# Kernel tuning notes

Measured on AMD Instinct MI355X. Metric: run time of the kernel, lower is better.

## Reference

```python
import jax, jax.numpy as jnp
import numpy as np

D_MODEL = 1024
N_HEADS = 16
HEAD_DIM = D_MODEL // N_HEADS
NEG_INF = -1e10


def setup_inputs() -> dict:
    key = jax.random.key(0)
    ks = jax.random.split(key, 6)
    B, S = 2, 2048
    x = jax.random.normal(ks[0], (B, S, D_MODEL), dtype=jnp.float32)
    mask = jnp.ones((B, S), dtype=jnp.int32)
    scale_w = 1.0 / np.sqrt(D_MODEL)
    Wq = jax.random.normal(ks[1], (D_MODEL, D_MODEL), dtype=jnp.float32) * scale_w
    Wk = jax.random.normal(ks[2], (D_MODEL, D_MODEL), dtype=jnp.float32) * scale_w
    Wv = jax.random.normal(ks[3], (D_MODEL, D_MODEL), dtype=jnp.float32) * scale_w
    Wo = jax.random.normal(ks[4], (D_MODEL, D_MODEL), dtype=jnp.float32) * scale_w
    bq = jnp.zeros((D_MODEL,), jnp.float32)
    bk = jnp.zeros((D_MODEL,), jnp.float32)
    bv = jnp.zeros((D_MODEL,), jnp.float32)
    bo = jnp.zeros((D_MODEL,), jnp.float32)
    return {"x": x, "mask": mask, "Wq": Wq, "bq": bq, "Wk": Wk, "bk": bk,
            "Wv": Wv, "bv": bv, "Wo": Wo, "bo": bo}


def reference(x, mask, Wq, bq, Wk, bk, Wv, bv, Wo, bo):
    B, S, _ = x.shape
    # Linear projections (torch Linear: y = x @ W.T + b)
    Q = x @ Wq.T + bq
    K = x @ Wk.T + bk
    V = x @ Wv.T + bv
    # [B, H, S, Dh]
    Q = Q.reshape(B, S, N_HEADS, HEAD_DIM).transpose(0, 2, 1, 3)
    K = K.reshape(B, S, N_HEADS, HEAD_DIM).transpose(0, 2, 1, 3)
    V = V.reshape(B, S, N_HEADS, HEAD_DIM).transpose(0, 2, 1, 3)
    scale = jnp.sqrt(jnp.float32(HEAD_DIM))
    energy = jnp.einsum('bhqd,bhkd->bhqk', Q, K) / scale  # [B,H,S,S]
    # mask: [B,S] -> broadcast over heads and query dim (keys masked)
    m = mask[:, None, None, :]  # [B,1,1,S]
    energy = jnp.where(m == 0, jnp.float32(NEG_INF), energy)
    attention = jax.nn.softmax(energy, axis=-1)
    # dropout in eval mode = identity
    out = jnp.einsum('bhqk,bhkd->bhqd', attention, V)  # [B,H,S,Dh]
    out = out.transpose(0, 2, 1, 3).reshape(B, S, D_MODEL)
    return out @ Wo.T + bo
```

## Files before the change

kernel.cpp:

```cpp
#include <hip/hip_runtime.h>
#include <hip/hip_bf16.h>

typedef __hip_bfloat16 bf16;
typedef __attribute__((ext_vector_type(8))) short s8v;
typedef __attribute__((ext_vector_type(4))) float f4v;

#define D_MODEL 1024
#define S_LEN   2048
#define BATCH   2
#define NH      16
#define HD      64
#define M_TOTAL 4096

__device__ __forceinline__ void gll16(const bf16* g, bf16* l) {
    __builtin_amdgcn_global_load_lds(
        (const __attribute__((address_space(1))) void*)g,
        (__attribute__((address_space(3))) void*)l, 16, 0, 0);
}

__global__ __launch_bounds__(256) void cvt_bf16x8(const float* __restrict__ s,
                                                  bf16* __restrict__ d, int n) {
    int i = (blockIdx.x * 256 + threadIdx.x) * 8;
    if (i < n) {
        float4 a = *(const float4*)(s + i);
        float4 b = *(const float4*)(s + i + 4);
        union { bf16 h[8]; uint4 u; } p;
        p.h[0] = __float2bfloat16(a.x); p.h[1] = __float2bfloat16(a.y);
        p.h[2] = __float2bfloat16(a.z); p.h[3] = __float2bfloat16(a.w);
        p.h[4] = __float2bfloat16(b.x); p.h[5] = __float2bfloat16(b.y);
        p.h[6] = __float2bfloat16(b.z); p.h[7] = __float2bfloat16(b.w);
        *(uint4*)(d + i) = p.u;
    }
}

struct WPtrs { const float* s0; const float* s1; const float* s2; const float* s3;
               bf16* d0; bf16* d1; bf16* d2; bf16* d3; };

__global__ __launch_bounds__(256) void cvt_w(WPtrs p) {
    const float* s; bf16* d;
    switch (blockIdx.y) {
        case 0:  s = p.s0; d = p.d0; break;
        case 1:  s = p.s1; d = p.d1; break;
        case 2:  s = p.s2; d = p.d2; break;
        default: s = p.s3; d = p.d3; break;
    }
    int i = (blockIdx.x * 256 + threadIdx.x) * 8;
    float4 a = *(const float4*)(s + i);
    float4 b = *(const float4*)(s + i + 4);
    union { bf16 h[8]; uint4 u; } q;
    q.h[0] = __float2bfloat16(a.x); q.h[1] = __float2bfloat16(a.y);
    q.h[2] = __float2bfloat16(a.z); q.h[3] = __float2bfloat16(a.w);
    q.h[4] = __float2bfloat16(b.x); q.h[5] = __float2bfloat16(b.y);
    q.h[6] = __float2bfloat16(b.z); q.h[7] = __float2bfloat16(b.w);
    *(uint4*)(d + i) = q.u;
}

template<int TM, int TN>
__device__ __forceinline__ void gemm_main(const bf16* __restrict__ A,
                                          const bf16* __restrict__ W,
                                          bf16* As, bf16* Bs,
                                          int bm, int bn,
                                          f4v (&acc)[TM/32][TN/32])
{
    constexpr int FM = TM / 32, FN = TN / 32;
    constexpr int CALLS_A = TM / 16, CALLS = (TM + TN) / 16, PW = CALLS / 4;
    const int t = threadIdx.x, wv = t >> 6, lane = t & 63;
    const int quad = lane >> 4, l15 = lane & 15;
    const int wm = (wv >> 1) * (TM / 2), wn = (wv & 1) * (TN / 2);
    const int lr = lane >> 2, lc = (lane & 3) * 8;

    const bf16* aptr[FM];
    const bf16* bptr[FN];
    #pragma unroll
    for (int i = 0; i < FM; ++i) aptr[i] = As + (wm + i * 16 + l15) * 32 + quad * 8;
    #pragma unroll
    for (int j = 0; j < FN; ++j) bptr[j] = Bs + (wn + j * 16 + l15) * 32 + quad * 8;

    for (int k0 = 0; k0 < D_MODEL; k0 += 32) {
        __syncthreads();
        #pragma unroll
        for (int c = 0; c < PW; ++c) {
            const int cc = wv * PW + c;
            if (cc < CALLS_A) {
                gll16(A + (size_t)(bm + cc * 16 + lr) * D_MODEL + k0 + lc,
                      As + cc * 16 * 32);
            } else {
                const int r2 = cc - CALLS_A;
                gll16(W + (size_t)(bn + r2 * 16 + lr) * D_MODEL + k0 + lc,
                      Bs + r2 * 16 * 32);
            }
        }
        __syncthreads();

        s8v af[FM], bfv[FN];
        #pragma unroll
        for (int i = 0; i < FM; ++i) af[i] = *(const s8v*)aptr[i];
        #pragma unroll
        for (int j = 0; j < FN; ++j) bfv[j] = *(const s8v*)bptr[j];
        #pragma unroll
        for (int i = 0; i < FM; ++i)
            #pragma unroll
            for (int j = 0; j < FN; ++j)
                acc[i][j] = __builtin_amdgcn_mfma_f32_16x16x32_bf16(af[i], bfv[j], acc[i][j], 0, 0, 0);
    }
}

__global__ __launch_bounds__(256) void gemm_qkv(
    const bf16* __restrict__ x,
    const bf16* __restrict__ Wq, const bf16* __restrict__ Wk, const bf16* __restrict__ Wv,
    const float* __restrict__ bq, const float* __restrict__ bk, const float* __restrict__ bv,
    bf16* __restrict__ Qb, bf16* __restrict__ Kb, bf16* __restrict__ Vtb)
{
    __shared__ __align__(16) bf16 As[128 * 32];
    __shared__ __align__(16) bf16 Bs[128 * 32];
    const int z = blockIdx.z;
    const bf16*  W    = (z == 0) ? Wq : (z == 1) ? Wk : Wv;
    const float* bias = (z == 0) ? bq : (z == 1) ? bk : bv;
    bf16*        out  = (z == 0) ? Qb : (z == 1) ? Kb : Vtb;
    const int bm = blockIdx.y * 128, bn = blockIdx.x * 128;

    f4v acc[4][4] = {};
    gemm_main<128, 128>(x, W, As, Bs, bm, bn, acc);

    const int t = threadIdx.x, wv = t >> 6, lane = t & 63;
    const int quad = lane >> 4, l15 = lane & 15;
    const int wm = (wv >> 1) * 64, wn = (wv & 1) * 64;
    #pragma unroll
    for (int j = 0; j < 4; ++j) {
        const int col = bn + wn + j * 16 + l15;
        const float bv_ = bias[col];
        const int h = col >> 6, d = col & 63;
        #pragma unroll
        for (int i = 0; i < 4; ++i) {
            #pragma unroll
            for (int r = 0; r < 4; ++r) {
                const int row = bm + wm + i * 16 + quad * 4 + r;
                const int b = row >> 11, s = row & 2047;
                const float v = acc[i][j][r] + bv_;
                size_t idx;
                if (z == 2) idx = (((size_t)(b * NH + h)) * HD + d) * S_LEN + s;
                else        idx = (((size_t)(b * NH + h)) * S_LEN + s) * HD + d;
                out[idx] = __float2bfloat16(v);
            }
        }
    }
}

__global__ __launch_bounds__(256) void gemm_out(
    const bf16* __restrict__ Ob, const bf16* __restrict__ Wo,
    const float* __restrict__ bo, float* __restrict__ out)
{
    __shared__ __align__(16) bf16 As[64 * 32];
    __shared__ __align__(16) bf16 Bs[128 * 32];
    const int bm = blockIdx.y * 64, bn = blockIdx.x * 128;

    f4v acc[2][4] = {};
    gemm_main<64, 128>(Ob, Wo, As, Bs, bm, bn, acc);

    const int t = threadIdx.x, wv = t >> 6, lane = t & 63;
    const int quad = lane >> 4, l15 = lane & 15;
    const int wm = (wv >> 1) * 32, wn = (wv & 1) * 64;
    #pragma unroll
    for (int j = 0; j < 4; ++j) {
        const int col = bn + wn + j * 16 + l15;
        const float bv_ = bo[col];
        #pragma unroll
        for (int i = 0; i < 2; ++i)
            #pragma unroll
            for (int r = 0; r < 4; ++r) {
                const int row = bm + wm + i * 16 + quad * 4 + r;
                out[(size_t)row * D_MODEL + col] = acc[i][j][r] + bv_;
            }
    }
}

__global__ __launch_bounds__(256) void attn_mfma(
    const bf16* __restrict__ Q, const bf16* __restrict__ K,
    const bf16* __restrict__ Vt, const int* __restrict__ mask,
    bf16* __restrict__ O)
{
    __shared__ __align__(16) bf16 Ks[64][72];
    __shared__ __align__(16) bf16 Vts[64][72];
    __shared__ __align__(16) bf16 Ps[4][16][72];
    __shared__ __align__(16) int  msk[64];

    const int t = threadIdx.x, wv = t >> 6, lane = t & 63;
    const int quad = lane >> 4, l15 = lane & 15;
    const int qt = blockIdx.x & 31, h = (blockIdx.x >> 5) & 15, b = blockIdx.x >> 9;
    const int q0 = qt * 64;
    const size_t qkbase = ((size_t)(b * NH + h)) * S_LEN * HD;
    const size_t vtbase = ((size_t)(b * NH + h)) * HD * S_LEN;

    const bf16* qrow = Q + qkbase + (size_t)(q0 + wv * 16 + l15) * HD;
    const s8v qf0 = *(const s8v*)(qrow + quad * 8);
    const s8v qf1 = *(const s8v*)(qrow + 32 + quad * 8);

    const int srow = t >> 2, scoff = (t & 3) * 16;

    float mprev = -1e30f, lsum = 0.f;
    f4v oacc[4] = {};

    for (int kt = 0; kt < S_LEN / 64; ++kt) {
        const int k0 = kt * 64;
        __syncthreads();
        {
            const uint4* kp = (const uint4*)(K  + qkbase + (size_t)(k0 + srow) * HD + scoff);
            const uint4* vp = (const uint4*)(Vt + vtbase + (size_t)srow * S_LEN + k0 + scoff);
            uint4 ka = kp[0], kb2 = kp[1];
            uint4 va = vp[0], vb2 = vp[1];
            *(uint4*)&Ks[srow][scoff]      = ka;
            *(uint4*)&Ks[srow][scoff + 8]  = kb2;
            *(uint4*)&Vts[srow][scoff]     = va;
            *(uint4*)&Vts[srow][scoff + 8] = vb2;
            if (t < 64) msk[t] = mask[b * S_LEN + k0 + t];
        }
        __syncthreads();

        f4v st[4];
        #pragma unroll
        for (int c = 0; c < 4; ++c) {
            s8v kf0 = *(const s8v*)&Ks[c * 16 + l15][quad * 8];
            s8v kf1 = *(const s8v*)&Ks[c * 16 + l15][32 + quad * 8];
            f4v z = {0.f, 0.f, 0.f, 0.f};
            z = __builtin_amdgcn_mfma_f32_16x16x32_bf16(kf0, qf0, z, 0, 0, 0);
            z = __builtin_amdgcn_mfma_f32_16x16x32_bf16(kf1, qf1, z, 0, 0, 0);
            st[c] = z;
        }

        float mt = -1e30f;
        #pragma unroll
        for (int c = 0; c < 4; ++c) {
            const int4 mk = *(const int4*)&msk[c * 16 + quad * 4];
            float v0 = st[c][0] * 0.125f; if (mk.x == 0) v0 = -1e10f;
            float v1 = st[c][1] * 0.125f; if (mk.y == 0) v1 = -1e10f;
            float v2 = st[c][2] * 0.125f; if (mk.z == 0) v2 = -1e10f;
            float v3 = st[c][3] * 0.125f; if (mk.w == 0) v3 = -1e10f;
            st[c][0] = v0; st[c][1] = v1; st[c][2] = v2; st[c][3] = v3;
            mt = fmaxf(mt, fmaxf(fmaxf(v0, v1), fmaxf(v2, v3)));
        }
        mt = fmaxf(mt, __shfl_xor(mt, 16, 64));
        mt = fmaxf(mt, __shfl_xor(mt, 32, 64));

        const float mn = fmaxf(mprev, mt);
        const float alpha = __expf(mprev - mn);
        mprev = mn;

        float ps = 0.f;
        #pragma unroll
        for (int c = 0; c < 4; ++c) {
            #pragma unroll
            for (int r = 0; r < 4; ++r) {
                const float p = __expf(st[c][r] - mn);
                st[c][r] = p;
                ps += p;
            }
        }
        ps += __shfl_xor(ps, 16, 64);
        ps += __shfl_xor(ps, 32, 64);
        lsum = lsum * alpha + ps;

        #pragma unroll
        for (int c = 0; c < 4; ++c) {
            union { bf16 h[4]; short4 s4; } pk;
            pk.h[0] = __float2bfloat16(st[c][0]);
            pk.h[1] = __float2bfloat16(st[c][1]);
            pk.h[2] = __float2bfloat16(st[c][2]);
            pk.h[3] = __float2bfloat16(st[c][3]);
            *(short4*)&Ps[wv][l15][c * 16 + quad * 4] = pk.s4;
        }

        float av[4];
        #pragma unroll
        for (int r = 0; r < 4; ++r) av[r] = __shfl(alpha, quad * 4 + r, 64);
        #pragma unroll
        for (int dt = 0; dt < 4; ++dt)
            #pragma unroll
            for (int r = 0; r < 4; ++r) oacc[dt][r] *= av[r];

        s8v pf0 = *(const s8v*)&Ps[wv][l15][quad * 8];
        s8v pf1 = *(const s8v*)&Ps[wv][l15][32 + quad * 8];
        #pragma unroll
        for (int dt = 0; dt < 4; ++dt) {
            s8v vf0 = *(const s8v*)&Vts[dt * 16 + l15][quad * 8];
            s8v vf1 = *(const s8v*)&Vts[dt * 16 + l15][32 + quad * 8];
            oacc[dt] = __builtin_amdgcn_mfma_f32_16x16x32_bf16(pf0, vf0, oacc[dt], 0, 0, 0);
            oacc[dt] = __builtin_amdgcn_mfma_f32_16x16x32_bf16(pf1, vf1, oacc[dt], 0, 0, 0);
        }
    }

    float linv[4];
    #pragma unroll
    for (int r = 0; r < 4; ++r) linv[r] = 1.f / __shfl(lsum, quad * 4 + r, 64);
    #pragma unroll
    for (int dt = 0; dt < 4; ++dt) {
        #pragma unroll
        for (int r = 0; r < 4; ++r) {
            const int s = q0 + wv * 16 + quad * 4 + r;
            const int col = h * 64 + dt * 16 + l15;
            O[((size_t)b * S_LEN + s) * D_MODEL + col] = __float2bfloat16(oacc[dt][r] * linv[r]);
        }
    }
}

extern "C" void kernel_launch(void* const* d_in, const int* in_sizes, int n_in,
                              void* d_out, int out_size, void* d_ws, size_t ws_size,
                              hipStream_t stream) {
    const float* x    = (const float*)d_in[0];
    const int*   mask = (const int*)  d_in[1];
    const float* Wq   = (const float*)d_in[2];
    const float* bq   = (const float*)d_in[3];
    const float* Wk   = (const float*)d_in[4];
    const float* bk   = (const float*)d_in[5];
    const float* Wv   = (const float*)d_in[6];
    const float* bv   = (const float*)d_in[7];
    const float* Wo   = (const float*)d_in[8];
    const float* bo   = (const float*)d_in[9];
    float* out = (float*)d_out;

    char* w = (char*)d_ws;
    bf16* xb  = (bf16*)w; w += (size_t)M_TOTAL * D_MODEL * 2;
    bf16* Wqb = (bf16*)w; w += (size_t)D_MODEL * D_MODEL * 2;
    bf16* Wkb = (bf16*)w; w += (size_t)D_MODEL * D_MODEL * 2;
    bf16* Wvb = (bf16*)w; w += (size_t)D_MODEL * D_MODEL * 2;
    bf16* Wob = (bf16*)w; w += (size_t)D_MODEL * D_MODEL * 2;
    bf16* Qb  = (bf16*)w; w += (size_t)M_TOTAL * D_MODEL * 2;
    bf16* Kb  = (bf16*)w; w += (size_t)M_TOTAL * D_MODEL * 2;
    bf16* Vtb = (bf16*)w; w += (size_t)M_TOTAL * D_MODEL * 2;
    bf16* Ob  = (bf16*)w; w += (size_t)M_TOTAL * D_MODEL * 2;

    const int nx = M_TOTAL * D_MODEL;
    cvt_bf16x8<<<nx / 2048, 256, 0, stream>>>(x, xb, nx);
    WPtrs wp = { Wq, Wk, Wv, Wo, Wqb, Wkb, Wvb, Wob };
    cvt_w<<<dim3(D_MODEL * D_MODEL / 2048, 4), 256, 0, stream>>>(wp);

    gemm_qkv<<<dim3(8, 32, 3), 256, 0, stream>>>(xb, Wqb, Wkb, Wvb, bq, bk, bv, Qb, Kb, Vtb);

    attn_mfma<<<BATCH * NH * (S_LEN / 64), 256, 0, stream>>>(Qb, Kb, Vtb, mask, Ob);

    gemm_out<<<dim3(8, 64), 256, 0, stream>>>(Ob, Wob, bo, out);
}
```

Before: 242.3 us.

## Prefetch K/V tiles, use exp2 with lazy rescaling, transpose V stores via LDS

The attention loop now loads the next K/V tile into registers while the current tile is being computed. The softmax folds log2(e) into the scale and uses exp2, turns the mask into an additive bias, and skips the rescale when the running max barely changes. Row-sum reductions are deferred until after the loop, and s_setprio is raised around the MFMA blocks. Separately, the V-transpose epilogue of the QKV GEMM is staged through LDS so global writes become coalesced 16-byte stores; this adds extra LDS use, which may lower occupancy.

New measurement: 233.2 us. -3.8%, faster.

```diff
diff --git a/kernel.cpp b/kernel.cpp
--- a/kernel.cpp
+++ b/kernel.cpp
@@ -113,6 +113,7 @@
 {
     __shared__ __align__(16) bf16 As[128 * 32];
     __shared__ __align__(16) bf16 Bs[128 * 32];
+    __shared__ __align__(16) bf16 Tw[4][64][72];
     const int z = blockIdx.z;
     const bf16*  W    = (z == 0) ? Wq : (z == 1) ? Wk : Wv;
     const float* bias = (z == 0) ? bq : (z == 1) ? bk : bv;
@@ -125,22 +126,48 @@
     const int t = threadIdx.x, wv = t >> 6, lane = t & 63;
     const int quad = lane >> 4, l15 = lane & 15;
     const int wm = (wv >> 1) * 64, wn = (wv & 1) * 64;
-    #pragma unroll
-    for (int j = 0; j < 4; ++j) {
-        const int col = bn + wn + j * 16 + l15;
-        const float bv_ = bias[col];
-        const int h = col >> 6, d = col & 63;
-        #pragma unroll
-        for (int i = 0; i < 4; ++i) {
-            #pragma unroll
-            for (int r = 0; r < 4; ++r) {
-                const int row = bm + wm + i * 16 + quad * 4 + r;
-                const int b = row >> 11, s = row & 2047;
-                const float v = acc[i][j][r] + bv_;
-                size_t idx;
-                if (z == 2) idx = (((size_t)(b * NH + h)) * HD + d) * S_LEN + s;
-                else        idx = (((size_t)(b * NH + h)) * S_LEN + s) * HD + d;
-                out[idx] = __float2bfloat16(v);
+
+    if (z == 2) {
+        #pragma unroll
+        for (int j = 0; j < 4; ++j) {
+            const int col = bn + wn + j * 16 + l15;
+            const float bv_ = bias[col];
+            #pragma unroll
+            for (int i = 0; i < 4; ++i) {
+                #pragma unroll
+                for (int rp = 0; rp < 4; rp += 2) {
+                    union { bf16 h[2]; unsigned u; } p2;
+                    p2.h[0] = __float2bfloat16(acc[i][j][rp]     + bv_);
+                    p2.h[1] = __float2bfloat16(acc[i][j][rp + 1] + bv_);
+                    *(unsigned*)&Tw[wv][j * 16 + l15][i * 16 + quad * 4 + rp] = p2.u;
+                }
+            }
+        }
+        const int bb = (bm + wm) >> 11, s0 = (bm + wm) & 2047;
+        #pragma unroll
+        for (int p = 0; p < 8; ++p) {
+            const int dl = p * 8 + (lane >> 3);
+            const int sl = (lane & 7) * 8;
+            const int col = bn + wn + dl;
+            const int h = col >> 6, d = col & 63;
+            uint4 v = *(const uint4*)&Tw[wv][dl][sl];
+            *(uint4*)&out[(((size_t)(bb * NH + h)) * HD + d) * S_LEN + s0 + sl] = v;
+        }
+    } else {
+        #pragma unroll
+        for (int j = 0; j < 4; ++j) {
+            const int col = bn + wn + j * 16 + l15;
+            const float bv_ = bias[col];
+            const int h = col >> 6, d = col & 63;
+            #pragma unroll
+            for (int i = 0; i < 4; ++i) {
+                #pragma unroll
+                for (int r = 0; r < 4; ++r) {
+                    const int row = bm + wm + i * 16 + quad * 4 + r;
+                    const int b = row >> 11, s = row & 2047;
+                    const float v = acc[i][j][r] + bv_;
+                    out[(((size_t)(b * NH + h)) * S_LEN + s) * HD + d] = __float2bfloat16(v);
+                }
             }
         }
     }
@@ -182,7 +209,7 @@
     __shared__ __align__(16) bf16 Ks[64][72];
     __shared__ __align__(16) bf16 Vts[64][72];
     __shared__ __align__(16) bf16 Ps[4][16][72];
-    __shared__ __align__(16) int  msk[64];
+    __shared__ float mb[64];
 
     const int t = threadIdx.x, wv = t >> 6, lane = t & 63;
     const int quad = lane >> 4, l15 = lane & 15;
@@ -191,32 +218,41 @@
     const size_t qkbase = ((size_t)(b * NH + h)) * S_LEN * HD;
     const size_t vtbase = ((size_t)(b * NH + h)) * HD * S_LEN;
 
+    const float KSC  = 0.125f * 1.44269504f;
+    const float THR2 = 8.0f * 1.44269504f;
+
     const bf16* qrow = Q + qkbase + (size_t)(q0 + wv * 16 + l15) * HD;
     const s8v qf0 = *(const s8v*)(qrow + quad * 8);
     const s8v qf1 = *(const s8v*)(qrow + 32 + quad * 8);
 
     const int srow = t >> 2, scoff = (t & 3) * 16;
 
+    uint4 kr0, kr1, vr0, vr1; int mr = 1;
+    auto LOADT = [&](int kt2) {
+        const int kk = kt2 * 64;
+        const uint4* kp = (const uint4*)(K  + qkbase + (size_t)(kk + srow) * HD + scoff);
+        const uint4* vp = (const uint4*)(Vt + vtbase + (size_t)srow * S_LEN + kk + scoff);
+        kr0 = kp[0]; kr1 = kp[1];
+        vr0 = vp[0]; vr1 = vp[1];
+        if (t < 64) mr = mask[b * S_LEN + kk + t];
+    };
+    LOADT(0);
+
     float mprev = -1e30f, lsum = 0.f;
     f4v oacc[4] = {};
 
     for (int kt = 0; kt < S_LEN / 64; ++kt) {
-        const int k0 = kt * 64;
         __syncthreads();
-        {
-            const uint4* kp = (const uint4*)(K  + qkbase + (size_t)(k0 + srow) * HD + scoff);
-            const uint4* vp = (const uint4*)(Vt + vtbase + (size_t)srow * S_LEN + k0 + scoff);
-            uint4 ka = kp[0], kb2 = kp[1];
-            uint4 va = vp[0], vb2 = vp[1];
-            *(uint4*)&Ks[srow][scoff]      = ka;
-            *(uint4*)&Ks[srow][scoff + 8]  = kb2;
-            *(uint4*)&Vts[srow][scoff]     = va;
-            *(uint4*)&Vts[srow][scoff + 8] = vb2;
-            if (t < 64) msk[t] = mask[b * S_LEN + k0 + t];
-        }
+        *(uint4*)&Ks[srow][scoff]       = kr0;
+        *(uint4*)&Ks[srow][scoff + 8]   = kr1;
+        *(uint4*)&Vts[srow][scoff]      = vr0;
+        *(uint4*)&Vts[srow][scoff + 8]  = vr1;
+        if (t < 64) mb[t] = mr ? 0.f : -1e30f;
         __syncthreads();
+        if (kt + 1 < S_LEN / 64) LOADT(kt + 1);
 
         f4v st[4];
+        __builtin_amdgcn_s_setprio(1);
         #pragma unroll
         for (int c = 0; c < 4; ++c) {
             s8v kf0 = *(const s8v*)&Ks[c * 16 + l15][quad * 8];
@@ -226,38 +262,48 @@
             z = __builtin_amdgcn_mfma_f32_16x16x32_bf16(kf1, qf1, z, 0, 0, 0);
             st[c] = z;
         }
+        __builtin_amdgcn_s_setprio(0);
 
         float mt = -1e30f;
         #pragma unroll
         for (int c = 0; c < 4; ++c) {
-            const int4 mk = *(const int4*)&msk[c * 16 + quad * 4];
-            float v0 = st[c][0] * 0.125f; if (mk.x == 0) v0 = -1e10f;
-            float v1 = st[c][1] * 0.125f; if (mk.y == 0) v1 = -1e10f;
-            float v2 = st[c][2] * 0.125f; if (mk.z == 0) v2 = -1e10f;
-            float v3 = st[c][3] * 0.125f; if (mk.w == 0) v3 = -1e10f;
+            const float4 mk = *(const float4*)&mb[c * 16 + quad * 4];
+            const float v0 = st[c][0] * KSC + mk.x;
+            const float v1 = st[c][1] * KSC + mk.y;
+            const float v2 = st[c][2] * KSC + mk.z;
+            const float v3 = st[c][3] * KSC + mk.w;
             st[c][0] = v0; st[c][1] = v1; st[c][2] = v2; st[c][3] = v3;
             mt = fmaxf(mt, fmaxf(fmaxf(v0, v1), fmaxf(v2, v3)));
         }
         mt = fmaxf(mt, __shfl_xor(mt, 16, 64));
         mt = fmaxf(mt, __shfl_xor(mt, 32, 64));
 
-        const float mn = fmaxf(mprev, mt);
-        const float alpha = __expf(mprev - mn);
-        mprev = mn;
+        float mn = mprev;
+        if (!__all(mt <= mprev + THR2)) {
+            mn = fmaxf(mprev, mt);
+            const float alpha = __builtin_amdgcn_exp2f(mprev - mn);
+            mprev = mn;
+            float av[4];
+            #pragma unroll
+            for (int r = 0; r < 4; ++r) av[r] = __shfl(alpha, quad * 4 + r, 64);
+            #pragma unroll
+            for (int dt = 0; dt < 4; ++dt)
+                #pragma unroll
+                for (int r = 0; r < 4; ++r) oacc[dt][r] *= av[r];
+            lsum *= alpha;
+        }
 
         float ps = 0.f;
         #pragma unroll
         for (int c = 0; c < 4; ++c) {
             #pragma unroll
             for (int r = 0; r < 4; ++r) {
-                const float p = __expf(st[c][r] - mn);
+                const float p = __builtin_amdgcn_exp2f(st[c][r] - mn);
                 st[c][r] = p;
                 ps += p;
             }
         }
-        ps += __shfl_xor(ps, 16, 64);
-        ps += __shfl_xor(ps, 32, 64);
-        lsum = lsum * alpha + ps;
+        lsum += ps;
 
         #pragma unroll
         for (int c = 0; c < 4; ++c) {
@@ -269,16 +315,9 @@
             *(short4*)&Ps[wv][l15][c * 16 + quad * 4] = pk.s4;
         }
 
-        float av[4];
-        #pragma unroll
-        for (int r = 0; r < 4; ++r) av[r] = __shfl(alpha, quad * 4 + r, 64);
-        #pragma unroll
-        for (int dt = 0; dt < 4; ++dt)
-            #pragma unroll
-            for (int r = 0; r < 4; ++r) oacc[dt][r] *= av[r];
-
         s8v pf0 = *(const s8v*)&Ps[wv][l15][quad * 8];
         s8v pf1 = *(const s8v*)&Ps[wv][l15][32 + quad * 8];
+        __builtin_amdgcn_s_setprio(1);
         #pragma unroll
         for (int dt = 0; dt < 4; ++dt) {
             s8v vf0 = *(const s8v*)&Vts[dt * 16 + l15][quad * 8];
@@ -286,8 +325,11 @@
             oacc[dt] = __builtin_amdgcn_mfma_f32_16x16x32_bf16(pf0, vf0, oacc[dt], 0, 0, 0);
             oacc[dt] = __builtin_amdgcn_mfma_f32_16x16x32_bf16(pf1, vf1, oacc[dt], 0, 0, 0);
         }
-    }
-
+        __builtin_amdgcn_s_setprio(0);
+    }
+
+    lsum += __shfl_xor(lsum, 16, 64);
+    lsum += __shfl_xor(lsum, 32, 64);
     float linv[4];
     #pragma unroll
     for (int r = 0; r < 4; ++r) linv[r] = 1.f / __shfl(lsum, quad * 4 + r, 64);
```
